# Kernel tuning notes

Hardware: AMD Instinct MI355X
Metric: run time of the kernel (lower is better)

The kernel has to match this reference:

```python
import jax, jax.numpy as jnp
import numpy as np

N_QUBITS = 12
N_LAYERS = 3
N_PARAMS = N_QUBITS * 3 * N_LAYERS  # 108
BATCH = 8192
DIM = 1 << N_QUBITS  # 4096


def _rx(theta):
    c = jnp.cos(theta / 2).astype(jnp.complex64)
    s = jnp.sin(theta / 2).astype(jnp.complex64)
    return jnp.stack([jnp.stack([c, -1j * s]), jnp.stack([-1j * s, c])])


def _ry(theta):
    c = jnp.cos(theta / 2).astype(jnp.complex64)
    s = jnp.sin(theta / 2).astype(jnp.complex64)
    return jnp.stack([jnp.stack([c, -s]), jnp.stack([s, c])])


def _rz(theta):
    e = jnp.exp(-1j * theta.astype(jnp.complex64) / 2)
    z = jnp.zeros((), jnp.complex64)
    return jnp.stack([jnp.stack([e, z]), jnp.stack([z, jnp.conj(e)])])


def _apply_1q(state, q, U):
    # state: (B,) + (2,)*n ; apply 2x2 gate U on wire q (axis q+1)
    s = jnp.moveaxis(state, q + 1, -1)
    s = s @ U.T
    return jnp.moveaxis(s, -1, q + 1)


def _cnot(state, c, t):
    # control wire c, target wire t (axes offset by 1 for batch dim)
    ca, ta = c + 1, t + 1
    s0 = jax.lax.index_in_dim(state, 0, ca, keepdims=False)
    s1 = jax.lax.index_in_dim(state, 1, ca, keepdims=False)
    ta2 = ta - 1 if ta > ca else ta  # target axis shifts after removing control axis
    s1 = jnp.flip(s1, axis=ta2)  # X on target (size-2 axis)
    return jnp.stack([s0, s1], axis=ca)


def setup_inputs() -> dict:
    key = jax.random.key(0)
    k1, k2 = jax.random.split(key)
    x = jax.random.normal(k1, (BATCH, DIM), dtype=jnp.float32)
    params = jax.random.normal(k2, (N_PARAMS,), dtype=jnp.float32) * 0.1
    return {"x": x, "params": params}


def reference(x, params):
    n = N_QUBITS
    B = x.shape[0]
    # AmplitudeEmbedding with normalize=True
    norm = jnp.linalg.norm(x, axis=1, keepdims=True)
    state = (x / norm).astype(jnp.complex64).reshape((B,) + (2,) * n)
    idx = 0
    for _ in range(N_LAYERS):
        for q in range(n):
            state = _apply_1q(state, q, _rx(params[idx])); idx += 1
            state = _apply_1q(state, q, _ry(params[idx])); idx += 1
            state = _apply_1q(state, q, _rz(params[idx])); idx += 1
        for q in range(n):
            state = _cnot(state, q, (q + 1) % n)
    # <Z_q> = P(q=0) - P(q=1)
    p = state.real ** 2 + state.imag ** 2  # (B,) + (2,)*n, float32
    outs = []
    for q in range(n):
        axes = tuple(a for a in range(1, n + 1) if a != q + 1)
        marg = jnp.sum(p, axis=axes)  # (B, 2)
        outs.append(marg[:, 0] - marg[:, 1])
    return jnp.stack(outs, axis=1)  # (B, n_qubits)
```

## Files before the change

kernel.cpp:

```cpp
#include <hip/hip_runtime.h>
#include <math.h>

#define NQ 12
#define DIM 4096
#define NGATES 36
#define NROUND 9

typedef float f32x2 __attribute__((ext_vector_type(2)));

constexpr unsigned swz(unsigned x) { return x ^ (x >> 4); }

struct Round {
  unsigned s[4];
  unsigned l[4];
  unsigned cbsw8[16];
};
struct PlanT {
  Round rd[NROUND];
  unsigned zsel[NQ];
};

constexpr PlanT make_plan() {
  PlanT P{};
  unsigned Mcol[NQ] = {}, Minv[NQ] = {};
  for (int i = 0; i < NQ; ++i) { Mcol[i] = 1u << i; Minv[i] = 1u << i; }
  unsigned gm[NGATES] = {}, gs[NGATES] = {};
  int g = 0;
  for (int L = 0; L < 3; ++L) {
    for (int q = 0; q < NQ; ++q) { int b = NQ - 1 - q; gm[g] = Mcol[b]; gs[g] = Minv[b]; ++g; }
    for (int q = 0; q < NQ; ++q) {
      int bc = NQ - 1 - q, bt = NQ - 1 - ((q + 1) % NQ);
      Mcol[bc] ^= Mcol[bt];
      Minv[bt] ^= Minv[bc];
    }
  }
  for (int r = 0; r < NROUND; ++r) {
    unsigned m[4], red[4];
    for (int k = 0; k < 4; ++k) { m[k] = gm[4*r+k]; red[k] = m[k]; P.rd[r].s[k] = gs[4*r+k]; }
    for (int a = 0; a < 4; ++a) {
      unsigned p = red[a] & (0u - red[a]);
      for (int b = a + 1; b < 4; ++b) if (red[b] & p) red[b] ^= red[a];
    }
    unsigned piv[4];
    for (int a = 0; a < 4; ++a) piv[a] = red[a] & (0u - red[a]);
    for (int a = 0; a < 4; ++a)
      for (int b = a + 1; b < 4; ++b)
        if (piv[a] > piv[b]) { unsigned tp = piv[a]; piv[a] = piv[b]; piv[b] = tp; }
    for (int a = 0; a < 4; ++a) P.rd[r].l[a] = piv[a] - 1u;
    for (int d = 0; d < 16; ++d) {
      unsigned c = 0;
      for (int k = 0; k < 4; ++k) if (d & (1 << k)) c ^= m[k];
      P.rd[r].cbsw8[d] = swz(c) << 3;
    }
  }
  for (int q = 0; q < NQ; ++q) P.zsel[q] = Minv[NQ - 1 - q];
  return P;
}

constexpr PlanT PLAN = make_plan();

__global__ void qc_prep(const float* __restrict__ params, f32x2* __restrict__ gpk) {
  int t = threadIdx.x;
  if (t < NGATES) {
    float h1 = params[3*t+0]*0.5f, h2 = params[3*t+1]*0.5f, h3 = params[3*t+2]*0.5f;
    float c1 = cosf(h1), s1 = sinf(h1);
    float c2 = cosf(h2), s2 = sinf(h2);
    float c3 = cosf(h3), s3 = sinf(h3);
    float a00r =  c2*c1, a00i =  s2*s1;
    float a01r = -s2*c1, a01i = -c2*s1;
    float a10r =  s2*c1, a10i = -c2*s1;
    float a11r =  c2*c1, a11i = -s2*s1;
    float u[8];
    u[0] = c3*a00r + s3*a00i;  u[1] = c3*a00i - s3*a00r;
    u[2] = c3*a01r + s3*a01i;  u[3] = c3*a01i - s3*a01r;
    u[4] = c3*a10r - s3*a10i;  u[5] = c3*a10i + s3*a10r;
    u[6] = c3*a11r - s3*a11i;  u[7] = c3*a11i + s3*a11r;
    f32x2* o = gpk + t*8;
#pragma unroll
    for (int k = 0; k < 4; ++k) {
      f32x2 a, b;
      a[0] =  u[2*k];   a[1] = u[2*k+1];
      b[0] = -u[2*k+1]; b[1] = u[2*k];
      o[2*k]   = a;
      o[2*k+1] = b;
    }
  }
}

__device__ __forceinline__ f32x2 blo(f32x2 a) { return __builtin_shufflevector(a, a, 0, 0); }
__device__ __forceinline__ f32x2 bhi(f32x2 a) { return __builtin_shufflevector(a, a, 1, 1); }

__global__ __launch_bounds__(256)
__attribute__((amdgpu_waves_per_eu(5, 5)))
void qc_main(const float* __restrict__ x, const f32x2* __restrict__ gpk,
             float* __restrict__ out) {
  __shared__ float2 sst[DIM];
  char* sb = (char*)sst;
  float* sf = (float*)sst;
  const int t = threadIdx.x;
  const long row = blockIdx.x;

  const float4* x4 = (const float4*)(x + (size_t)row * DIM);
  float ssq = 0.f;
#pragma unroll
  for (int k = 0; k < 4; ++k) {
    float4 a = x4[t + 256*k];
    int j0 = 4*(t + 256*k);
    *(float2*)(sb + (swz((unsigned)j0)     << 3)) = make_float2(a.x, 0.f);
    *(float2*)(sb + (swz((unsigned)(j0+1)) << 3)) = make_float2(a.y, 0.f);
    *(float2*)(sb + (swz((unsigned)(j0+2)) << 3)) = make_float2(a.z, 0.f);
    *(float2*)(sb + (swz((unsigned)(j0+3)) << 3)) = make_float2(a.w, 0.f);
    ssq += a.x*a.x + a.y*a.y + a.z*a.z + a.w*a.w;
  }
#pragma unroll
  for (int off = 32; off > 0; off >>= 1) ssq += __shfl_down(ssq, off, 64);
  __syncthreads();

#pragma unroll 1
  for (int r = 0; r < NROUND; ++r) {
    const unsigned s0 = PLAN.rd[r].s[0], sA = PLAN.rd[r].s[1];
    const unsigned sB = PLAN.rd[r].s[2], sC = PLAN.rd[r].s[3];
    const unsigned l0 = PLAN.rd[r].l[0], l1 = PLAN.rd[r].l[1];
    const unsigned l2 = PLAN.rd[r].l[2], l3 = PLAN.rd[r].l[3];
    unsigned cb[16];
#pragma unroll
    for (int d = 0; d < 16; ++d) cb[d] = PLAN.rd[r].cbsw8[d];

    unsigned j = (unsigned)t;
    j = ((j & ~l0) << 1) | (j & l0);
    j = ((j & ~l1) << 1) | (j & l1);
    j = ((j & ~l2) << 1) | (j & l2);
    j = ((j & ~l3) << 1) | (j & l3);
    unsigned adj8 = 0;
    adj8 ^= (unsigned)(-(int)(__popc(j & s0) & 1)) & cb[1];
    adj8 ^= (unsigned)(-(int)(__popc(j & sA) & 1)) & cb[2];
    adj8 ^= (unsigned)(-(int)(__popc(j & sB) & 1)) & cb[4];
    adj8 ^= (unsigned)(-(int)(__popc(j & sC) & 1)) & cb[8];
    const unsigned base8 = ((j ^ (j >> 4)) << 3) ^ adj8;

    f32x2 v[16];
#pragma unroll
    for (int d = 0; d < 16; ++d)
      v[d] = *(const f32x2*)(sb + (base8 ^ cb[d]));

#pragma unroll
    for (int st = 0; st < 4; ++st) {
      const f32x2* cp = gpk + (r * 4 + st) * 8;
      const f32x2 c0 = cp[0], c1 = cp[1], c2 = cp[2], c3 = cp[3];
      const f32x2 c4 = cp[4], c5 = cp[5], c6 = cp[6], c7 = cp[7];
#pragma unroll
      for (int d = 0; d < 16; ++d) {
        if (!(d & (1 << st))) {
          const int d1 = d | (1 << st);
          const f32x2 a0 = v[d], a1 = v[d1];
          f32x2 o0 = c0 * blo(a0);
          o0 += c1 * bhi(a0);
          o0 += c2 * blo(a1);
          o0 += c3 * bhi(a1);
          f32x2 o1 = c4 * blo(a0);
          o1 += c5 * bhi(a0);
          o1 += c6 * blo(a1);
          o1 += c7 * bhi(a1);
          v[d] = o0; v[d1] = o1;
        }
      }
    }
#pragma unroll
    for (int d = 0; d < 16; ++d)
      *(f32x2*)(sb + (base8 ^ cb[d])) = v[d];
    __syncthreads();
  }

  const unsigned mbase8 = (((16u * (unsigned)t) ^ (unsigned)t) << 3);
  float p[16];
#pragma unroll
  for (int c = 0; c < 16; ++c) {
    f32x2 v = *(const f32x2*)(sb + (mbase8 ^ ((unsigned)c << 3)));
    f32x2 sq = v * v;
    p[c] = sq[0] + sq[1];
  }
#pragma unroll
  for (int b = 0; b < 4; ++b) {
#pragma unroll
    for (int c = 0; c < 16; ++c) {
      if (!(c & (1 << b))) {
        const int c1 = c | (1 << b);
        float u = p[c], v = p[c1];
        p[c] = u + v; p[c1] = u - v;
      }
    }
  }
  float zs[NQ];
#pragma unroll
  for (int q = 0; q < NQ; ++q) {
    const unsigned m = PLAN.zsel[q];
    const float v = p[m & 15u];
    const int sgn = __popc((unsigned)t & (m >> 4)) & 1;
    zs[q] = sgn ? -v : v;
  }
#pragma unroll
  for (int q = 0; q < NQ; ++q) {
#pragma unroll
    for (int off = 32; off > 0; off >>= 1) zs[q] += __shfl_down(zs[q], off, 64);
  }
  __syncthreads();
  const int w = t >> 6;
  if ((t & 63) == 0) {
#pragma unroll
    for (int q = 0; q < NQ; ++q) sf[w*NQ + q] = zs[q];
    sf[48 + w] = ssq;
  }
  __syncthreads();
  if (t < NQ) {
    const float den = sf[48] + sf[49] + sf[50] + sf[51];
    const float tot = sf[t] + sf[NQ + t] + sf[2*NQ + t] + sf[3*NQ + t];
    out[row * NQ + t] = tot / den;
  }
}

extern "C" void kernel_launch(void* const* d_in, const int* in_sizes, int n_in,
                              void* d_out, int out_size, void* d_ws, size_t ws_size,
                              hipStream_t stream) {
  const float* x = (const float*)d_in[0];
  const float* params = (const float*)d_in[1];
  float* out = (float*)d_out;
  f32x2* gpk = (f32x2*)d_ws;
  const int nrows = in_sizes[0] / DIM;
  qc_prep<<<dim3(1), dim3(64), 0, stream>>>(params, gpk);
  qc_main<<<dim3(nrows), dim3(256), 0, stream>>>(x, gpk, out);
}
```

Measured before the change: 349.3 us.

## Pair gate rounds per wave-local subspace to halve block barriers, fuse prep

Groups consecutive 4-gate rounds into pairs where each wave owns a closed subspace of amplitudes, so two rounds run back-to-back without a block-wide barrier; this roughly halves the __syncthreads count. Gate matrices are now computed in every block from params with sincosf and broadcast with readlane instead of a separate prep kernel and global loads. The layout plan is checked at compile time for rank and delta validity. The cost is redundant trig per block and extra readlane and address math per subround.

```diff
diff --git a/kernel.cpp b/kernel.cpp
--- a/kernel.cpp
+++ b/kernel.cpp
@@ -4,24 +4,40 @@
 #define NQ 12
 #define DIM 4096
 #define NGATES 36
-#define NROUND 9
+#define NPAIR 5
 
 typedef float f32x2 __attribute__((ext_vector_type(2)));
 
 constexpr unsigned swz(unsigned x) { return x ^ (x >> 4); }
 
-struct Round {
-  unsigned s[4];
-  unsigned l[4];
-  unsigned cbsw8[16];
+struct PairT {
+  unsigned lbA[6], lbB[6];
+  unsigned wb[2];
+  unsigned cbA8[16], cbB8[16];
+  unsigned sA[4], sB[4];
 };
 struct PlanT {
-  Round rd[NROUND];
+  PairT pr[NPAIR];
   unsigned zsel[NQ];
+  bool ok;
 };
+
+constexpr int rnk12(const unsigned* v) {
+  unsigned r[12] = {};
+  for (int i = 0; i < 12; ++i) r[i] = v[i];
+  int rk = 0;
+  for (int a = 0; a < 12; ++a) {
+    if (!r[a]) continue;
+    unsigned piv = r[a] & (0u - r[a]);
+    ++rk;
+    for (int b = a + 1; b < 12; ++b) if (r[b] & piv) r[b] ^= r[a];
+  }
+  return rk;
+}
 
 constexpr PlanT make_plan() {
   PlanT P{};
+  P.ok = true;
   unsigned Mcol[NQ] = {}, Minv[NQ] = {};
   for (int i = 0; i < NQ; ++i) { Mcol[i] = 1u << i; Minv[i] = 1u << i; }
   unsigned gm[NGATES] = {}, gs[NGATES] = {};
@@ -34,71 +50,100 @@
       Minv[bt] ^= Minv[bc];
     }
   }
-  for (int r = 0; r < NROUND; ++r) {
-    unsigned m[4], red[4];
-    for (int k = 0; k < 4; ++k) { m[k] = gm[4*r+k]; red[k] = m[k]; P.rd[r].s[k] = gs[4*r+k]; }
-    for (int a = 0; a < 4; ++a) {
-      unsigned p = red[a] & (0u - red[a]);
-      for (int b = a + 1; b < 4; ++b) if (red[b] & p) red[b] ^= red[a];
-    }
-    unsigned piv[4];
-    for (int a = 0; a < 4; ++a) piv[a] = red[a] & (0u - red[a]);
-    for (int a = 0; a < 4; ++a)
-      for (int b = a + 1; b < 4; ++b)
-        if (piv[a] > piv[b]) { unsigned tp = piv[a]; piv[a] = piv[b]; piv[b] = tp; }
-    for (int a = 0; a < 4; ++a) P.rd[r].l[a] = piv[a] - 1u;
+  for (int p = 0; p < NPAIR; ++p) {
+    const int gb = 8 * p;
+    const bool hasB = (p < 4);
+    unsigned mA[4] = {}, mB[4] = {};
+    for (int k = 0; k < 4; ++k) { mA[k] = gm[gb + k]; P.pr[p].sA[k] = gs[gb + k]; }
+    if (hasB)
+      for (int k = 0; k < 4; ++k) { mB[k] = gm[gb + 4 + k]; P.pr[p].sB[k] = gs[gb + 4 + k]; }
+    unsigned rows[8] = {mA[0], mA[1], mA[2], mA[3], mB[0], mB[1], mB[2], mB[3]};
+    const int nr = hasB ? 8 : 4;
+    unsigned pivmask = 0;
+    for (int a = 0; a < nr; ++a) {
+      unsigned piv = rows[a] & (0u - rows[a]);
+      pivmask |= piv;
+      for (int b = a + 1; b < nr; ++b) if (rows[b] & piv) rows[b] ^= rows[a];
+    }
+    unsigned fr[12] = {}; int nf = 0;
+    for (int bit = 0; bit < 12; ++bit)
+      if (!((pivmask >> bit) & 1u)) fr[nf++] = 1u << bit;
+    if (hasB) {
+      if (nf != 4) P.ok = false;
+      for (int k = 0; k < 4; ++k) { P.pr[p].lbA[k] = mB[k]; P.pr[p].lbB[k] = mA[k]; }
+      P.pr[p].lbA[4] = fr[0]; P.pr[p].lbA[5] = fr[1];
+      P.pr[p].lbB[4] = fr[0]; P.pr[p].lbB[5] = fr[1];
+      P.pr[p].wb[0] = fr[2];  P.pr[p].wb[1] = fr[3];
+    } else {
+      if (nf != 8) P.ok = false;
+      for (int k = 0; k < 6; ++k) { P.pr[p].lbA[k] = fr[k]; P.pr[p].lbB[k] = fr[k]; }
+      P.pr[p].wb[0] = fr[6]; P.pr[p].wb[1] = fr[7];
+    }
     for (int d = 0; d < 16; ++d) {
-      unsigned c = 0;
-      for (int k = 0; k < 4; ++k) if (d & (1 << k)) c ^= m[k];
-      P.rd[r].cbsw8[d] = swz(c) << 3;
-    }
+      unsigned cA = 0, cB = 0;
+      for (int k = 0; k < 4; ++k) if (d & (1 << k)) { cA ^= mA[k]; cB ^= mB[k]; }
+      P.pr[p].cbA8[d] = swz(cA) << 3;
+      P.pr[p].cbB8[d] = swz(cB) << 3;
+    }
+    unsigned vA[12] = {mA[0], mA[1], mA[2], mA[3],
+                       P.pr[p].lbA[0], P.pr[p].lbA[1], P.pr[p].lbA[2],
+                       P.pr[p].lbA[3], P.pr[p].lbA[4], P.pr[p].lbA[5],
+                       P.pr[p].wb[0], P.pr[p].wb[1]};
+    if (rnk12(vA) != 12) P.ok = false;
+    if (hasB) {
+      unsigned vB[12] = {mB[0], mB[1], mB[2], mB[3],
+                         P.pr[p].lbB[0], P.pr[p].lbB[1], P.pr[p].lbB[2],
+                         P.pr[p].lbB[3], P.pr[p].lbB[4], P.pr[p].lbB[5],
+                         P.pr[p].wb[0], P.pr[p].wb[1]};
+      if (rnk12(vB) != 12) P.ok = false;
+    }
+    for (int i = 0; i < 4; ++i)
+      for (int k = 0; k < 4; ++k) {
+        if ((__builtin_popcount(mA[i] & P.pr[p].sA[k]) & 1) != (i == k ? 1 : 0)) P.ok = false;
+        if (hasB && (__builtin_popcount(mB[i] & P.pr[p].sB[k]) & 1) != (i == k ? 1 : 0)) P.ok = false;
+      }
   }
   for (int q = 0; q < NQ; ++q) P.zsel[q] = Minv[NQ - 1 - q];
   return P;
 }
 
 constexpr PlanT PLAN = make_plan();
-
-__global__ void qc_prep(const float* __restrict__ params, f32x2* __restrict__ gpk) {
-  int t = threadIdx.x;
-  if (t < NGATES) {
-    float h1 = params[3*t+0]*0.5f, h2 = params[3*t+1]*0.5f, h3 = params[3*t+2]*0.5f;
-    float c1 = cosf(h1), s1 = sinf(h1);
-    float c2 = cosf(h2), s2 = sinf(h2);
-    float c3 = cosf(h3), s3 = sinf(h3);
-    float a00r =  c2*c1, a00i =  s2*s1;
-    float a01r = -s2*c1, a01i = -c2*s1;
-    float a10r =  s2*c1, a10i = -c2*s1;
-    float a11r =  c2*c1, a11i = -s2*s1;
-    float u[8];
-    u[0] = c3*a00r + s3*a00i;  u[1] = c3*a00i - s3*a00r;
-    u[2] = c3*a01r + s3*a01i;  u[3] = c3*a01i - s3*a01r;
-    u[4] = c3*a10r - s3*a10i;  u[5] = c3*a10i + s3*a10r;
-    u[6] = c3*a11r - s3*a11i;  u[7] = c3*a11i + s3*a11r;
-    f32x2* o = gpk + t*8;
-#pragma unroll
-    for (int k = 0; k < 4; ++k) {
-      f32x2 a, b;
-      a[0] =  u[2*k];   a[1] = u[2*k+1];
-      b[0] = -u[2*k+1]; b[1] = u[2*k];
-      o[2*k]   = a;
-      o[2*k+1] = b;
-    }
-  }
-}
+static_assert(PLAN.ok, "circuit plan failed rank/delta validation");
 
 __device__ __forceinline__ f32x2 blo(f32x2 a) { return __builtin_shufflevector(a, a, 0, 0); }
 __device__ __forceinline__ f32x2 bhi(f32x2 a) { return __builtin_shufflevector(a, a, 1, 1); }
+__device__ __forceinline__ float rdlane(float v, int lane) {
+  return __builtin_bit_cast(float, __builtin_amdgcn_readlane(__builtin_bit_cast(int, v), lane));
+}
 
 __global__ __launch_bounds__(256)
 __attribute__((amdgpu_waves_per_eu(5, 5)))
-void qc_main(const float* __restrict__ x, const f32x2* __restrict__ gpk,
+void qc_main(const float* __restrict__ x, const float* __restrict__ params,
              float* __restrict__ out) {
   __shared__ float2 sst[DIM];
   char* sb = (char*)sst;
   float* sf = (float*)sst;
   const int t = threadIdx.x;
   const long row = blockIdx.x;
+
+  float cf[8];
+  {
+    const int l = t & 63;
+    const int g0 = l < NGATES ? l : 0;
+    float h1 = params[3*g0+0]*0.5f, h2 = params[3*g0+1]*0.5f, h3 = params[3*g0+2]*0.5f;
+    float c1, s1, c2, s2, c3, s3;
+    sincosf(h1, &s1, &c1);
+    sincosf(h2, &s2, &c2);
+    sincosf(h3, &s3, &c3);
+    float a00r =  c2*c1, a00i =  s2*s1;
+    float a01r = -s2*c1, a01i = -c2*s1;
+    float a10r =  s2*c1, a10i = -c2*s1;
+    float a11r =  c2*c1, a11i = -s2*s1;
+    cf[0] = c3*a00r + s3*a00i;  cf[1] = c3*a00i - s3*a00r;
+    cf[2] = c3*a01r + s3*a01i;  cf[3] = c3*a01i - s3*a01r;
+    cf[4] = c3*a10r - s3*a10i;  cf[5] = c3*a10i + s3*a10r;
+    cf[6] = c3*a11r - s3*a11i;  cf[7] = c3*a11i + s3*a11r;
+  }
 
   const float4* x4 = (const float4*)(x + (size_t)row * DIM);
   float ssq = 0.f;
@@ -116,38 +161,33 @@
   for (int off = 32; off > 0; off >>= 1) ssq += __shfl_down(ssq, off, 64);
   __syncthreads();
 
-#pragma unroll 1
-  for (int r = 0; r < NROUND; ++r) {
-    const unsigned s0 = PLAN.rd[r].s[0], sA = PLAN.rd[r].s[1];
-    const unsigned sB = PLAN.rd[r].s[2], sC = PLAN.rd[r].s[3];
-    const unsigned l0 = PLAN.rd[r].l[0], l1 = PLAN.rd[r].l[1];
-    const unsigned l2 = PLAN.rd[r].l[2], l3 = PLAN.rd[r].l[3];
-    unsigned cb[16];
-#pragma unroll
-    for (int d = 0; d < 16; ++d) cb[d] = PLAN.rd[r].cbsw8[d];
-
-    unsigned j = (unsigned)t;
-    j = ((j & ~l0) << 1) | (j & l0);
-    j = ((j & ~l1) << 1) | (j & l1);
-    j = ((j & ~l2) << 1) | (j & l2);
-    j = ((j & ~l3) << 1) | (j & l3);
+  auto subround = [&](const unsigned* lb, const unsigned* cb8, const unsigned* sel,
+                      int gbase, unsigned wbase) {
+    const unsigned l = (unsigned)t & 63u;
+    unsigned jp = wbase;
+#pragma unroll
+    for (int k = 0; k < 6; ++k)
+      jp ^= (unsigned)(-(int)((l >> k) & 1u)) & lb[k];
     unsigned adj8 = 0;
-    adj8 ^= (unsigned)(-(int)(__popc(j & s0) & 1)) & cb[1];
-    adj8 ^= (unsigned)(-(int)(__popc(j & sA) & 1)) & cb[2];
-    adj8 ^= (unsigned)(-(int)(__popc(j & sB) & 1)) & cb[4];
-    adj8 ^= (unsigned)(-(int)(__popc(j & sC) & 1)) & cb[8];
-    const unsigned base8 = ((j ^ (j >> 4)) << 3) ^ adj8;
+    adj8 ^= (unsigned)(-(int)(__popc(jp & sel[0]) & 1)) & cb8[1];
+    adj8 ^= (unsigned)(-(int)(__popc(jp & sel[1]) & 1)) & cb8[2];
+    adj8 ^= (unsigned)(-(int)(__popc(jp & sel[2]) & 1)) & cb8[4];
+    adj8 ^= (unsigned)(-(int)(__popc(jp & sel[3]) & 1)) & cb8[8];
+    const unsigned base8 = ((jp ^ (jp >> 4)) << 3) ^ adj8;
 
     f32x2 v[16];
 #pragma unroll
     for (int d = 0; d < 16; ++d)
-      v[d] = *(const f32x2*)(sb + (base8 ^ cb[d]));
-
+      v[d] = *(const f32x2*)(sb + (base8 ^ cb8[d]));
 #pragma unroll
     for (int st = 0; st < 4; ++st) {
-      const f32x2* cp = gpk + (r * 4 + st) * 8;
-      const f32x2 c0 = cp[0], c1 = cp[1], c2 = cp[2], c3 = cp[3];
-      const f32x2 c4 = cp[4], c5 = cp[5], c6 = cp[6], c7 = cp[7];
+      const int gg = gbase + st;
+      float u0 = rdlane(cf[0], gg), u1 = rdlane(cf[1], gg);
+      float u2 = rdlane(cf[2], gg), u3 = rdlane(cf[3], gg);
+      float u4 = rdlane(cf[4], gg), u5 = rdlane(cf[5], gg);
+      float u6 = rdlane(cf[6], gg), u7 = rdlane(cf[7], gg);
+      const f32x2 c0 = {u0, u1}, c1 = {-u1, u0}, c2 = {u2, u3}, c3 = {-u3, u2};
+      const f32x2 c4 = {u4, u5}, c5 = {-u5, u4}, c6 = {u6, u7}, c7 = {-u7, u6};
 #pragma unroll
       for (int d = 0; d < 16; ++d) {
         if (!(d & (1 << st))) {
@@ -167,7 +207,16 @@
     }
 #pragma unroll
     for (int d = 0; d < 16; ++d)
-      *(f32x2*)(sb + (base8 ^ cb[d])) = v[d];
+      *(f32x2*)(sb + (base8 ^ cb8[d])) = v[d];
+  };
+
+#pragma unroll 1
+  for (int p = 0; p < NPAIR; ++p) {
+    const unsigned wbase = ((t & 64) ? PLAN.pr[p].wb[0] : 0u)
+                         ^ ((t & 128) ? PLAN.pr[p].wb[1] : 0u);
+    subround(PLAN.pr[p].lbA, PLAN.pr[p].cbA8, PLAN.pr[p].sA, 8 * p, wbase);
+    if (p < 4)
+      subround(PLAN.pr[p].lbB, PLAN.pr[p].cbB8, PLAN.pr[p].sB, 8 * p + 4, wbase);
     __syncthreads();
   }
 
@@ -224,8 +273,6 @@
   const float* x = (const float*)d_in[0];
   const float* params = (const float*)d_in[1];
   float* out = (float*)d_out;
-  f32x2* gpk = (f32x2*)d_ws;
   const int nrows = in_sizes[0] / DIM;
-  qc_prep<<<dim3(1), dim3(64), 0, stream>>>(params, gpk);
-  qc_main<<<dim3(nrows), dim3(256), 0, stream>>>(x, gpk, out);
-}
+  qc_main<<<dim3(nrows), dim3(256), 0, stream>>>(x, params, out);
+}
```

New measurement: 440.6 us. 1.26x slower.
